# Kernel optimization log

Hardware: AMD Instinct MI355X
Metric: run time of the kernel (lower is better)

Reference implementation:

```python
import jax, jax.numpy as jnp
import numpy as np

COST_CLASS = 1.0
COST_COORD = 1.0
ALPHA = 0.25
GAMMA = 2.0
EPS = 1e-8
B, N = 4, 512


def setup_inputs() -> dict:
    key = jax.random.key(0)
    k1, k2, k3 = jax.random.split(key, 3)
    return {
        "pred_logits": jax.random.normal(k1, (B, N), dtype=jnp.float32),
        "pred_points": jax.random.uniform(k2, (B, N, 2), dtype=jnp.float32),
        "gt_points": jax.random.uniform(k3, (B, N, 2), dtype=jnp.float32),
        "gt_mask": jnp.ones((B, N), dtype=bool),
    }


def _cost_matrix(pred_logits, pred_points, gt_points):
    # focal-style classification cost, depends only on the prediction -> column-constant
    prob = jax.nn.sigmoid(pred_logits)                       # [B, N]
    neg = (1.0 - ALPHA) * prob ** GAMMA * (-jnp.log(1.0 - prob + EPS))
    pos = ALPHA * (1.0 - prob) ** GAMMA * (-jnp.log(prob + EPS))
    cost_class = (pos - neg)[:, :, None]                     # [B, N, 1]
    # L1 cdist between pred_points and gt_points
    cost_coord = jnp.sum(
        jnp.abs(pred_points[:, :, None, :] - gt_points[:, None, :, :]), axis=-1
    )                                                        # [B, N, N]
    return COST_CLASS * cost_class + COST_COORD * cost_coord


def _lsa(cost):
    # Jonker-Volgenant shortest augmenting path (e-maxx Hungarian), square, minimization.
    c = np.asarray(cost, dtype=np.float64)
    n = c.shape[0]
    INF = 1e18
    u = np.zeros(n + 1)
    v = np.zeros(n + 1)
    p = np.zeros(n + 1, dtype=np.int64)   # p[j] = row matched to column j (1-based)
    way = np.zeros(n + 1, dtype=np.int64)
    for i in range(1, n + 1):
        p[0] = i
        j0 = 0
        minv = np.full(n + 1, INF)
        used = np.zeros(n + 1, dtype=bool)
        while True:
            used[j0] = True
            i0 = p[j0]
            cur = c[i0 - 1] - u[i0] - v[1:]
            nu = ~used[1:]
            mv = minv[1:]
            wy = way[1:]
            upd = nu & (cur < mv)
            mv[upd] = cur[upd]
            wy[upd] = j0
            cand = np.where(nu, mv, INF)
            j1 = int(np.argmin(cand)) + 1
            delta = cand[j1 - 1]
            u[p[used]] += delta
            v[used] -= delta
            mv[nu] -= delta
            j0 = j1
            if p[j0] == 0:
                break
        while j0:
            j1 = int(way[j0])
            p[j0] = int(p[j1])
            j0 = j1
    col_of_row = np.empty(n, dtype=np.int64)
    col_of_row[p[1:] - 1] = np.arange(n)
    return np.arange(n), col_of_row


def reference(pred_logits, pred_points, gt_points, gt_mask):
    C = _cost_matrix(pred_logits, pred_points, gt_points)   # [B, N, N]
    mask = np.asarray(gt_mask)
    assert mask.all(), "reference assumes all gt slots valid (static shapes)"
    Cn = np.asarray(jax.device_get(C))
    pred_idx, gt_idx = [], []
    for b in range(Cn.shape[0]):
        r, c = _lsa(Cn[b])
        pred_idx.append(r)
        gt_idx.append(c)
    pred_idx = jnp.asarray(np.stack(pred_idx))
    gt_idx = jnp.asarray(np.stack(gt_idx))
    return pred_idx, gt_idx, C
```

## Files before the change

kernel.cpp:

```cpp
#include <hip/hip_runtime.h>
#include <math.h>

constexpr int B_ = 4;
constexpr int N_ = 512;

__device__ __forceinline__ float cephes_expf(float xin) {
#pragma clang fp contract(off)
    float x = fminf(xin, 88.3762626647950f);
    x = fmaxf(x, -88.3762626647949f);
    float fx = x * 1.44269504088896341f;
    fx = fx + 0.5f;
    fx = floorf(fx);
    float tmp = fx * 0.693359375f;
    float z0  = fx * -2.12194440e-4f;
    float r = x - tmp;
    r = r - z0;
    float zz = r * r;
    float y = 1.9875691500E-4f;
    y = y * r + 1.3981999507E-3f;
    y = y * r + 8.3334519073E-3f;
    y = y * r + 4.1665795894E-2f;
    y = y * r + 1.6666665459E-1f;
    y = y * r + 5.0000001201E-1f;
    y = y * zz + r;
    y = y + 1.0f;
    int n = (int)fx;
    float p2n = __uint_as_float((unsigned)(n + 0x7f) << 23);
    float res = y * p2n;
    return fmaxf(res, xin);
}

__device__ __forceinline__ float cephes_logf(float t) {
#pragma clang fp contract(off)
    float xx = fmaxf(t, 1.17549435e-38f);
    unsigned u = __float_as_uint(xx);
    int e_i = (int)(u >> 23) - 0x7f;
    float e = (float)e_i + 1.0f;
    float m = __uint_as_float((u & 0x807fffffu) | 0x3f000000u);
    int mask = (m < 0.707106781186547524f);
    float tmp1 = mask ? m : 0.0f;
    float x = m - 1.0f;
    e = e - (mask ? 1.0f : 0.0f);
    x = x + tmp1;
    float z = x * x;
    float y = 7.0376836292E-2f;
    y = y * x + -1.1514610310E-1f;
    y = y * x + 1.1676998740E-1f;
    y = y * x + -1.2420140846E-1f;
    y = y * x + 1.4249322787E-1f;
    y = y * x + -1.6668057665E-1f;
    y = y * x + 2.0000714765E-1f;
    y = y * x + -2.4999993993E-1f;
    y = y * x + 3.3333331174E-1f;
    y = y * x;
    y = y * z;
    y = e * -2.12194440e-4f + y;
    y = y - z * 0.5f;
    float res = x + y;
    res = res + e * 0.693359375f;
    return res;
}

__global__ __launch_bounds__(256) void class_cost_kernel(
    const float* __restrict__ logits, float* __restrict__ cc_out)
{
#pragma clang fp contract(off)
    int idx = blockIdx.x * 256 + threadIdx.x;
    if (idx >= B_ * N_) return;
    float x    = logits[idx];
    float e    = cephes_expf(-x);
    float prob = 1.0f / (1.0f + e);
    float om   = 1.0f - prob;
    float p2   = prob * prob;
    float o2   = om * om;
    float lneg = cephes_logf(om   + 1e-8f);
    float lpos = cephes_logf(prob + 1e-8f);
    float neg  = (0.75f * p2) * (-lneg);
    float pos  = (0.25f * o2) * (-lpos);
    cc_out[idx] = pos - neg;
}

__global__ __launch_bounds__(512) void cost_kernel(
    const float* __restrict__ cc,
    const float* __restrict__ pred_pts,
    const float* __restrict__ gt_pts,
    float* __restrict__ C)
{
    int blk = blockIdx.x;
    int b = blk >> 9;
    int i = blk & (N_ - 1);
    int j = threadIdx.x;

    const float2* pp2 = reinterpret_cast<const float2*>(pred_pts);
    const float2* gp2 = reinterpret_cast<const float2*>(gt_pts);
    float2 pp = pp2[b * N_ + i];
    float2 gp = gp2[b * N_ + j];
    float coord = fabsf(pp.x - gp.x) + fabsf(pp.y - gp.y);

    C[(size_t)b * N_ * N_ + (size_t)i * N_ + j] = cc[blk] + coord;
}

template<int CTRL>
__device__ __forceinline__ uint32_t dpp32(uint32_t x) {
    return (uint32_t)__builtin_amdgcn_update_dpp((int)x, (int)x, CTRL, 0xF, 0xF, false);
}

__device__ __forceinline__ uint64_t f64_key(double d) {
    uint64_t b = (uint64_t)__double_as_longlong(d);
    return b ^ ((b >> 63) ? 0xFFFFFFFFFFFFFFFFull : 0x8000000000000000ull);
}

__device__ __forceinline__ double readlane_f64(double d, int lane) {
    unsigned long long ll = (unsigned long long)__double_as_longlong(d);
    unsigned lo = (unsigned)__builtin_amdgcn_readlane((int)(unsigned)ll, lane);
    unsigned hi = (unsigned)__builtin_amdgcn_readlane((int)(unsigned)(ll >> 32), lane);
    return __longlong_as_double((long long)(((unsigned long long)hi << 32) | lo));
}

#define VSTEP(CTRL) {                                                          \
    uint32_t lo_o = dpp32<CTRL>(klo);                                          \
    uint32_t hi_o = dpp32<CTRL>(khi);                                          \
    uint64_t ko = ((uint64_t)hi_o << 32) | lo_o;                               \
    uint64_t kc = ((uint64_t)khi  << 32) | klo;                                \
    bool lt = (ko < kc);                                                       \
    klo = lt ? lo_o : klo; khi = lt ? hi_o : khi;                              \
}

__global__ __launch_bounds__(64) void solve_kernel(
    const float* __restrict__ C,
    float* __restrict__ pred_idx,
    float* __restrict__ gt_idx)
{
    const int b = blockIdx.x;
    const int t = threadIdx.x;
    const float*  Cs  = C + (size_t)b * N_ * N_;
    const float4* rp0 = reinterpret_cast<const float4*>(Cs);

    float4 pa = rp0[2 * t];
    float4 pb = rp0[2 * t + 1];

    {
        float w0 = 0.f, w1 = 0.f, w2 = 0.f, w3 = 0.f,
              w4 = 0.f, w5 = 0.f, w6 = 0.f, w7 = 0.f;
        for (int it = 0; it < 128; it += 8) {
            w0 += Cs[(t + 64 * (it + 0)) * 32];
            w1 += Cs[(t + 64 * (it + 1)) * 32];
            w2 += Cs[(t + 64 * (it + 2)) * 32];
            w3 += Cs[(t + 64 * (it + 3)) * 32];
            w4 += Cs[(t + 64 * (it + 4)) * 32];
            w5 += Cs[(t + 64 * (it + 5)) * 32];
            w6 += Cs[(t + 64 * (it + 6)) * 32];
            w7 += Cs[(t + 64 * (it + 7)) * 32];
        }
        float wsum = ((w0 + w1) + (w2 + w3)) + ((w4 + w5) + (w6 + w7));
        __asm__ volatile("" : : "v"(wsum));
    }

    double u0=0.0,u1=0.0,u2=0.0,u3=0.0,u4=0.0,u5=0.0,u6=0.0,u7=0.0;
    double v0=0.0,v1=0.0,v2=0.0,v3=0.0,v4=0.0,v5=0.0,v6=0.0,v7=0.0;
    int    p0=-1,p1=-1,p2=-1,p3=-1,p4=-1,p5=-1,p6=-1,p7=-1;

    #pragma unroll
    for (int k = 0; k < 8; ++k)
        pred_idx[b * N_ + t + 64 * k] = (float)(t + 64 * k);

    auto read_u_at = [&](int r) -> double {
        int sl = r & 7, ln = r >> 3;
        double x0 = (sl & 1) ? u1 : u0;
        double x1 = (sl & 1) ? u3 : u2;
        double x2 = (sl & 1) ? u5 : u4;
        double x3 = (sl & 1) ? u7 : u6;
        double y0 = (sl & 2) ? x1 : x0;
        double y1 = (sl & 2) ? x3 : x2;
        double z  = (sl & 4) ? y1 : y0;
        return readlane_f64(z, ln);
    };

    for (int i = 0; i < N_; ++i) {
        unsigned used_m  = 0u;
        unsigned chain_m = (t == (i >> 3)) ? (1u << (i & 7)) : 0u;
        double urow = read_u_at(i);
        float4 ca = pa, cb = pb;

        {
            int nxt = (i + 1 < N_) ? (i + 1) : i;
            const float4* rpn = rp0 + (nxt << 7);
            pa = rpn[2 * t];
            pb = rpn[2 * t + 1];
        }

        for (;;) {
            uint64_t q0 = (used_m & 0x01u) ? ~0ull : f64_key(((double)ca.x - urow) - v0);
            uint64_t q1 = (used_m & 0x02u) ? ~0ull : f64_key(((double)ca.y - urow) - v1);
            uint64_t q2 = (used_m & 0x04u) ? ~0ull : f64_key(((double)ca.z - urow) - v2);
            uint64_t q3 = (used_m & 0x08u) ? ~0ull : f64_key(((double)ca.w - urow) - v3);
            uint64_t q4 = (used_m & 0x10u) ? ~0ull : f64_key(((double)cb.x - urow) - v4);
            uint64_t q5 = (used_m & 0x20u) ? ~0ull : f64_key(((double)cb.y - urow) - v5);
            uint64_t q6 = (used_m & 0x40u) ? ~0ull : f64_key(((double)cb.z - urow) - v6);
            uint64_t q7 = (used_m & 0x80u) ? ~0ull : f64_key(((double)cb.w - urow) - v7);

            uint64_t ka = (q1 < q0) ? q1 : q0;  uint32_t sa = (q1 < q0) ? 1u : 0u;
            uint64_t kb = (q3 < q2) ? q3 : q2;  uint32_t sb = (q3 < q2) ? 3u : 2u;
            uint64_t kx = (q5 < q4) ? q5 : q4;  uint32_t sx = (q5 < q4) ? 5u : 4u;
            uint64_t kd = (q7 < q6) ? q7 : q6;  uint32_t sd = (q7 < q6) ? 7u : 6u;
            uint64_t ke = (kb < ka) ? kb : ka;  uint32_t se = (kb < ka) ? sb : sa;
            uint64_t kf = (kd < kx) ? kd : kx;  uint32_t sf = (kd < kx) ? sd : sx;
            uint64_t bk = (kf < ke) ? kf : ke;  uint32_t bslot = (kf < ke) ? sf : se;

            uint32_t klo = (uint32_t)bk, khi = (uint32_t)(bk >> 32);
            VSTEP(0x111) VSTEP(0x112) VSTEP(0x114)
            VSTEP(0x118) VSTEP(0x142) VSTEP(0x143)
            uint32_t Mlo = (uint32_t)__builtin_amdgcn_readlane((int)klo, 63);
            uint32_t Mhi = (uint32_t)__builtin_amdgcn_readlane((int)khi, 63);
            uint64_t M = ((uint64_t)Mhi << 32) | Mlo;

            unsigned long long tied = __ballot(bk == M);
            int lane1 = (int)__builtin_ctzll(tied);
            int slot1 = __builtin_amdgcn_readlane((int)bslot, lane1);

            int a0 = (slot1 & 1) ? p1 : p0;
            int a1 = (slot1 & 1) ? p3 : p2;
            int a2 = (slot1 & 1) ? p5 : p4;
            int a3 = (slot1 & 1) ? p7 : p6;
            int b0 = (slot1 & 2) ? a1 : a0;
            int b1 = (slot1 & 2) ? a3 : a2;
            int zz = (slot1 & 4) ? b1 : b0;
            int owner = __builtin_amdgcn_readlane(zz, lane1);

            uint64_t db = (M >> 63) ? (M ^ 0x8000000000000000ull) : ~M;
            double delta = __longlong_as_double((long long)db);

            if (owner < 0) {
                u0 += (chain_m & 0x01u) ? delta : 0.0;
                u1 += (chain_m & 0x02u) ? delta : 0.0;
                u2 += (chain_m & 0x04u) ? delta : 0.0;
                u3 += (chain_m & 0x08u) ? delta : 0.0;
                u4 += (chain_m & 0x10u) ? delta : 0.0;
                u5 += (chain_m & 0x20u) ? delta : 0.0;
                u6 += (chain_m & 0x40u) ? delta : 0.0;
                u7 += (chain_m & 0x80u) ? delta : 0.0;
                v0 -= (used_m  & 0x01u) ? delta : 0.0;
                v1 -= (used_m  & 0x02u) ? delta : 0.0;
                v2 -= (used_m  & 0x04u) ? delta : 0.0;
                v3 -= (used_m  & 0x08u) ? delta : 0.0;
                v4 -= (used_m  & 0x10u) ? delta : 0.0;
                v5 -= (used_m  & 0x20u) ? delta : 0.0;
                v6 -= (used_m  & 0x40u) ? delta : 0.0;
                v7 -= (used_m  & 0x80u) ? delta : 0.0;
                bool mine = (t == lane1);
                p0 = (mine && slot1 == 0) ? i : p0;
                p1 = (mine && slot1 == 1) ? i : p1;
                p2 = (mine && slot1 == 2) ? i : p2;
                p3 = (mine && slot1 == 3) ? i : p3;
                p4 = (mine && slot1 == 4) ? i : p4;
                p5 = (mine && slot1 == 5) ? i : p5;
                p6 = (mine && slot1 == 6) ? i : p6;
                p7 = (mine && slot1 == 7) ? i : p7;
                break;
            }

            {
                const float4* rp = rp0 + (owner << 7);
                ca = rp[2 * t];
                cb = rp[2 * t + 1];
            }
            urow = read_u_at(owner);

            u0 += (chain_m & 0x01u) ? delta : 0.0;
            u1 += (chain_m & 0x02u) ? delta : 0.0;
            u2 += (chain_m & 0x04u) ? delta : 0.0;
            u3 += (chain_m & 0x08u) ? delta : 0.0;
            u4 += (chain_m & 0x10u) ? delta : 0.0;
            u5 += (chain_m & 0x20u) ? delta : 0.0;
            u6 += (chain_m & 0x40u) ? delta : 0.0;
            u7 += (chain_m & 0x80u) ? delta : 0.0;
            v0 -= (used_m  & 0x01u) ? delta : 0.0;
            v1 -= (used_m  & 0x02u) ? delta : 0.0;
            v2 -= (used_m  & 0x04u) ? delta : 0.0;
            v3 -= (used_m  & 0x08u) ? delta : 0.0;
            v4 -= (used_m  & 0x10u) ? delta : 0.0;
            v5 -= (used_m  & 0x20u) ? delta : 0.0;
            v6 -= (used_m  & 0x40u) ? delta : 0.0;
            v7 -= (used_m  & 0x80u) ? delta : 0.0;

            used_m  |= (t == lane1)        ? (1u << slot1)       : 0u;
            chain_m |= (t == (owner >> 3)) ? (1u << (owner & 7)) : 0u;
        }
    }

    const int j0 = t << 3;
    gt_idx[b * N_ + p0] = (float)(j0);
    gt_idx[b * N_ + p1] = (float)(j0 + 1);
    gt_idx[b * N_ + p2] = (float)(j0 + 2);
    gt_idx[b * N_ + p3] = (float)(j0 + 3);
    gt_idx[b * N_ + p4] = (float)(j0 + 4);
    gt_idx[b * N_ + p5] = (float)(j0 + 5);
    gt_idx[b * N_ + p6] = (float)(j0 + 6);
    gt_idx[b * N_ + p7] = (float)(j0 + 7);
}

extern "C" void kernel_launch(void* const* d_in, const int* in_sizes, int n_in,
                              void* d_out, int out_size, void* d_ws, size_t ws_size,
                              hipStream_t stream)
{
    const float* logits   = (const float*)d_in[0];
    const float* pred_pts = (const float*)d_in[1];
    const float* gt_pts   = (const float*)d_in[2];

    float* out      = (float*)d_out;
    float* pred_idx = out;
    float* gt_idx   = out + B_ * N_;
    float* C        = out + 2 * B_ * N_;
    float* cc       = (float*)d_ws;

    class_cost_kernel<<<(B_ * N_ + 255) / 256, 256, 0, stream>>>(logits, cc);
    cost_kernel<<<B_ * N_, N_, 0, stream>>>(cc, pred_pts, gt_pts, C);
    solve_kernel<<<B_, 64, 0, stream>>>(C, pred_idx, gt_idx);
}
```

Before: 2.036 ms.

## Recompute cost rows in registers inside solver and use 32-bit two-stage wave min

```diff
diff --git a/kernel.cpp b/kernel.cpp
--- a/kernel.cpp
+++ b/kernel.cpp
@@ -104,10 +104,12 @@
 __device__ __forceinline__ uint32_t dpp32(uint32_t x) {
     return (uint32_t)__builtin_amdgcn_update_dpp((int)x, (int)x, CTRL, 0xF, 0xF, false);
 }
-
-__device__ __forceinline__ uint64_t f64_key(double d) {
-    uint64_t b = (uint64_t)__double_as_longlong(d);
-    return b ^ ((b >> 63) ? 0xFFFFFFFFFFFFFFFFull : 0x8000000000000000ull);
+#define UMINSTEP(X, CTRL) { uint32_t o_ = dpp32<CTRL>(X); X = (o_ < X) ? o_ : X; }
+
+__device__ __forceinline__ uint32_t wave_umin_lane63(uint32_t x) {
+    UMINSTEP(x, 0x111) UMINSTEP(x, 0x112) UMINSTEP(x, 0x114)
+    UMINSTEP(x, 0x118) UMINSTEP(x, 0x142) UMINSTEP(x, 0x143)
+    return x;
 }
 
 __device__ __forceinline__ double readlane_f64(double d, int lane) {
@@ -117,44 +119,27 @@
     return __longlong_as_double((long long)(((unsigned long long)hi << 32) | lo));
 }
 
-#define VSTEP(CTRL) {                                                          \
-    uint32_t lo_o = dpp32<CTRL>(klo);                                          \
-    uint32_t hi_o = dpp32<CTRL>(khi);                                          \
-    uint64_t ko = ((uint64_t)hi_o << 32) | lo_o;                               \
-    uint64_t kc = ((uint64_t)khi  << 32) | klo;                                \
-    bool lt = (ko < kc);                                                       \
-    klo = lt ? lo_o : klo; khi = lt ? hi_o : khi;                              \
-}
-
 __global__ __launch_bounds__(64) void solve_kernel(
-    const float* __restrict__ C,
+    const float* __restrict__ cc_in,
+    const float* __restrict__ pred_pts,
+    const float* __restrict__ gt_pts,
     float* __restrict__ pred_idx,
     float* __restrict__ gt_idx)
 {
     const int b = blockIdx.x;
     const int t = threadIdx.x;
-    const float*  Cs  = C + (size_t)b * N_ * N_;
-    const float4* rp0 = reinterpret_cast<const float4*>(Cs);
-
-    float4 pa = rp0[2 * t];
-    float4 pb = rp0[2 * t + 1];
-
-    {
-        float w0 = 0.f, w1 = 0.f, w2 = 0.f, w3 = 0.f,
-              w4 = 0.f, w5 = 0.f, w6 = 0.f, w7 = 0.f;
-        for (int it = 0; it < 128; it += 8) {
-            w0 += Cs[(t + 64 * (it + 0)) * 32];
-            w1 += Cs[(t + 64 * (it + 1)) * 32];
-            w2 += Cs[(t + 64 * (it + 2)) * 32];
-            w3 += Cs[(t + 64 * (it + 3)) * 32];
-            w4 += Cs[(t + 64 * (it + 4)) * 32];
-            w5 += Cs[(t + 64 * (it + 5)) * 32];
-            w6 += Cs[(t + 64 * (it + 6)) * 32];
-            w7 += Cs[(t + 64 * (it + 7)) * 32];
-        }
-        float wsum = ((w0 + w1) + (w2 + w3)) + ((w4 + w5) + (w6 + w7));
-        __asm__ volatile("" : : "v"(wsum));
-    }
+
+    const float2* pq = reinterpret_cast<const float2*>(pred_pts) + b * N_;
+    const float2* gq = reinterpret_cast<const float2*>(gt_pts)   + b * N_;
+    const float*  cq = cc_in + b * N_;
+    const int base = t << 3;
+
+    float2 r0 = pq[base + 0], r1 = pq[base + 1], r2 = pq[base + 2], r3 = pq[base + 3];
+    float2 r4 = pq[base + 4], r5 = pq[base + 5], r6 = pq[base + 6], r7 = pq[base + 7];
+    float2 g0 = gq[base + 0], g1 = gq[base + 1], g2 = gq[base + 2], g3 = gq[base + 3];
+    float2 g4 = gq[base + 4], g5 = gq[base + 5], g6 = gq[base + 6], g7 = gq[base + 7];
+    float  c0 = cq[base + 0], c1 = cq[base + 1], c2 = cq[base + 2], c3 = cq[base + 3];
+    float  c4 = cq[base + 4], c5 = cq[base + 5], c6 = cq[base + 6], c7 = cq[base + 7];
 
     double u0=0.0,u1=0.0,u2=0.0,u3=0.0,u4=0.0,u5=0.0,u6=0.0,u7=0.0;
     double v0=0.0,v1=0.0,v2=0.0,v3=0.0,v4=0.0,v5=0.0,v6=0.0,v7=0.0;
@@ -164,69 +149,108 @@
     for (int k = 0; k < 8; ++k)
         pred_idx[b * N_ + t + 64 * k] = (float)(t + 64 * k);
 
-    auto read_u_at = [&](int r) -> double {
-        int sl = r & 7, ln = r >> 3;
-        double x0 = (sl & 1) ? u1 : u0;
-        double x1 = (sl & 1) ? u3 : u2;
-        double x2 = (sl & 1) ? u5 : u4;
-        double x3 = (sl & 1) ? u7 : u6;
-        double y0 = (sl & 2) ? x1 : x0;
-        double y1 = (sl & 2) ? x3 : x2;
-        double z  = (sl & 4) ? y1 : y0;
-        return readlane_f64(z, ln);
-    };
+    #define SEL8F(sl, x0,x1,x2,x3,x4,x5,x6,x7, out) {                      \
+        float a0_=((sl)&1)?(x1):(x0), a1_=((sl)&1)?(x3):(x2);              \
+        float a2_=((sl)&1)?(x5):(x4), a3_=((sl)&1)?(x7):(x6);              \
+        float b0_=((sl)&2)?a1_:a0_,   b1_=((sl)&2)?a3_:a2_;                \
+        out = ((sl)&4)?b1_:b0_; }
+    #define SEL8I(sl, x0,x1,x2,x3,x4,x5,x6,x7, out) {                      \
+        int a0_=((sl)&1)?(x1):(x0), a1_=((sl)&1)?(x3):(x2);                \
+        int a2_=((sl)&1)?(x5):(x4), a3_=((sl)&1)?(x7):(x6);                \
+        int b0_=((sl)&2)?a1_:a0_,   b1_=((sl)&2)?a3_:a2_;                  \
+        out = ((sl)&4)?b1_:b0_; }
+    #define SEL8D(sl, x0,x1,x2,x3,x4,x5,x6,x7, out) {                      \
+        double a0_=((sl)&1)?(x1):(x0), a1_=((sl)&1)?(x3):(x2);             \
+        double a2_=((sl)&1)?(x5):(x4), a3_=((sl)&1)?(x7):(x6);             \
+        double b0_=((sl)&2)?a1_:a0_,   b1_=((sl)&2)?a3_:a2_;               \
+        out = ((sl)&4)?b1_:b0_; }
+
+    float px_r, py_r, cc_r; double urow;
+    #define ROW_SCALARS(r) {                                               \
+        int sl_ = (r) & 7, ln_ = (r) >> 3;                                 \
+        float sx_, sy_, sc_; double su_;                                   \
+        SEL8F(sl_, r0.x,r1.x,r2.x,r3.x,r4.x,r5.x,r6.x,r7.x, sx_);          \
+        SEL8F(sl_, r0.y,r1.y,r2.y,r3.y,r4.y,r5.y,r6.y,r7.y, sy_);          \
+        SEL8F(sl_, c0,c1,c2,c3,c4,c5,c6,c7, sc_);                          \
+        SEL8D(sl_, u0,u1,u2,u3,u4,u5,u6,u7, su_);                          \
+        px_r = __uint_as_float((unsigned)__builtin_amdgcn_readlane(        \
+                   (int)__float_as_uint(sx_), ln_));                       \
+        py_r = __uint_as_float((unsigned)__builtin_amdgcn_readlane(        \
+                   (int)__float_as_uint(sy_), ln_));                       \
+        cc_r = __uint_as_float((unsigned)__builtin_amdgcn_readlane(        \
+                   (int)__float_as_uint(sc_), ln_));                       \
+        urow = readlane_f64(su_, ln_); }
+
+    const float INF32 = __uint_as_float(0x7F800000u);
 
     for (int i = 0; i < N_; ++i) {
         unsigned used_m  = 0u;
         unsigned chain_m = (t == (i >> 3)) ? (1u << (i & 7)) : 0u;
-        double urow = read_u_at(i);
-        float4 ca = pa, cb = pb;
-
-        {
-            int nxt = (i + 1 < N_) ? (i + 1) : i;
-            const float4* rpn = rp0 + (nxt << 7);
-            pa = rpn[2 * t];
-            pb = rpn[2 * t + 1];
-        }
+        ROW_SCALARS(i);
 
         for (;;) {
-            uint64_t q0 = (used_m & 0x01u) ? ~0ull : f64_key(((double)ca.x - urow) - v0);
-            uint64_t q1 = (used_m & 0x02u) ? ~0ull : f64_key(((double)ca.y - urow) - v1);
-            uint64_t q2 = (used_m & 0x04u) ? ~0ull : f64_key(((double)ca.z - urow) - v2);
-            uint64_t q3 = (used_m & 0x08u) ? ~0ull : f64_key(((double)ca.w - urow) - v3);
-            uint64_t q4 = (used_m & 0x10u) ? ~0ull : f64_key(((double)cb.x - urow) - v4);
-            uint64_t q5 = (used_m & 0x20u) ? ~0ull : f64_key(((double)cb.y - urow) - v5);
-            uint64_t q6 = (used_m & 0x40u) ? ~0ull : f64_key(((double)cb.z - urow) - v6);
-            uint64_t q7 = (used_m & 0x80u) ? ~0ull : f64_key(((double)cb.w - urow) - v7);
-
-            uint64_t ka = (q1 < q0) ? q1 : q0;  uint32_t sa = (q1 < q0) ? 1u : 0u;
-            uint64_t kb = (q3 < q2) ? q3 : q2;  uint32_t sb = (q3 < q2) ? 3u : 2u;
-            uint64_t kx = (q5 < q4) ? q5 : q4;  uint32_t sx = (q5 < q4) ? 5u : 4u;
-            uint64_t kd = (q7 < q6) ? q7 : q6;  uint32_t sd = (q7 < q6) ? 7u : 6u;
-            uint64_t ke = (kb < ka) ? kb : ka;  uint32_t se = (kb < ka) ? sb : sa;
-            uint64_t kf = (kd < kx) ? kd : kx;  uint32_t sf = (kd < kx) ? sd : sx;
-            uint64_t bk = (kf < ke) ? kf : ke;  uint32_t bslot = (kf < ke) ? sf : se;
-
-            uint32_t klo = (uint32_t)bk, khi = (uint32_t)(bk >> 32);
-            VSTEP(0x111) VSTEP(0x112) VSTEP(0x114)
-            VSTEP(0x118) VSTEP(0x142) VSTEP(0x143)
-            uint32_t Mlo = (uint32_t)__builtin_amdgcn_readlane((int)klo, 63);
-            uint32_t Mhi = (uint32_t)__builtin_amdgcn_readlane((int)khi, 63);
+#pragma clang fp contract(off)
+            float w0 = cc_r + (fabsf(px_r - g0.x) + fabsf(py_r - g0.y));
+            float w1 = cc_r + (fabsf(px_r - g1.x) + fabsf(py_r - g1.y));
+            float w2 = cc_r + (fabsf(px_r - g2.x) + fabsf(py_r - g2.y));
+            float w3 = cc_r + (fabsf(px_r - g3.x) + fabsf(py_r - g3.y));
+            float w4 = cc_r + (fabsf(px_r - g4.x) + fabsf(py_r - g4.y));
+            float w5 = cc_r + (fabsf(px_r - g5.x) + fabsf(py_r - g5.y));
+            float w6 = cc_r + (fabsf(px_r - g6.x) + fabsf(py_r - g6.y));
+            float w7 = cc_r + (fabsf(px_r - g7.x) + fabsf(py_r - g7.y));
+            w0 = (used_m & 0x01u) ? INF32 : w0;
+            w1 = (used_m & 0x02u) ? INF32 : w1;
+            w2 = (used_m & 0x04u) ? INF32 : w2;
+            w3 = (used_m & 0x08u) ? INF32 : w3;
+            w4 = (used_m & 0x10u) ? INF32 : w4;
+            w5 = (used_m & 0x20u) ? INF32 : w5;
+            w6 = (used_m & 0x40u) ? INF32 : w6;
+            w7 = (used_m & 0x80u) ? INF32 : w7;
+
+            double d0 = ((double)w0 - urow) - v0;
+            double d1 = ((double)w1 - urow) - v1;
+            double d2 = ((double)w2 - urow) - v2;
+            double d3 = ((double)w3 - urow) - v3;
+            double d4 = ((double)w4 - urow) - v4;
+            double d5 = ((double)w5 - urow) - v5;
+            double d6 = ((double)w6 - urow) - v6;
+            double d7 = ((double)w7 - urow) - v7;
+
+            double  ka = (d1 < d0) ? d1 : d0;  uint32_t sa = (d1 < d0) ? 1u : 0u;
+            double  kb = (d3 < d2) ? d3 : d2;  uint32_t sb = (d3 < d2) ? 3u : 2u;
+            double  kx = (d5 < d4) ? d5 : d4;  uint32_t sx = (d5 < d4) ? 5u : 4u;
+            double  kd = (d7 < d6) ? d7 : d6;  uint32_t sd = (d7 < d6) ? 7u : 6u;
+            double  ke = (kb < ka) ? kb : ka;  uint32_t se = (kb < ka) ? sb : sa;
+            double  kf = (kd < kx) ? kd : kx;  uint32_t sf = (kd < kx) ? sd : sx;
+            double  bv = (kf < ke) ? kf : ke;  uint32_t bslot = (kf < ke) ? sf : se;
+
+            uint64_t kb64 = (uint64_t)__double_as_longlong(bv);
+            kb64 ^= (kb64 >> 63) ? 0xFFFFFFFFFFFFFFFFull : 0x8000000000000000ull;
+            uint32_t khi = (uint32_t)(kb64 >> 32);
+            uint32_t klo = (uint32_t)kb64;
+
+            int own_pre;
+            SEL8I(bslot, p0,p1,p2,p3,p4,p5,p6,p7, own_pre);
+
+            uint32_t Mhi = (uint32_t)__builtin_amdgcn_readlane(
+                               (int)wave_umin_lane63(khi), 63);
+            unsigned long long tied_hi = __ballot(khi == Mhi);
+
+            int lane1; uint32_t Mlo;
+            if (__builtin_popcountll(tied_hi) == 1) {
+                lane1 = (int)__builtin_ctzll(tied_hi);
+                Mlo = (uint32_t)__builtin_amdgcn_readlane((int)klo, lane1);
+            } else {
+                uint32_t kl2 = (khi == Mhi) ? klo : 0xFFFFFFFFu;
+                Mlo = (uint32_t)__builtin_amdgcn_readlane(
+                          (int)wave_umin_lane63(kl2), 63);
+                lane1 = (int)__builtin_ctzll(__ballot(khi == Mhi && klo == Mlo));
+            }
+
+            int slot1 = __builtin_amdgcn_readlane((int)bslot, lane1);
+            int owner = __builtin_amdgcn_readlane(own_pre, lane1);
+
             uint64_t M = ((uint64_t)Mhi << 32) | Mlo;
-
-            unsigned long long tied = __ballot(bk == M);
-            int lane1 = (int)__builtin_ctzll(tied);
-            int slot1 = __builtin_amdgcn_readlane((int)bslot, lane1);
-
-            int a0 = (slot1 & 1) ? p1 : p0;
-            int a1 = (slot1 & 1) ? p3 : p2;
-            int a2 = (slot1 & 1) ? p5 : p4;
-            int a3 = (slot1 & 1) ? p7 : p6;
-            int b0 = (slot1 & 2) ? a1 : a0;
-            int b1 = (slot1 & 2) ? a3 : a2;
-            int zz = (slot1 & 4) ? b1 : b0;
-            int owner = __builtin_amdgcn_readlane(zz, lane1);
-
             uint64_t db = (M >> 63) ? (M ^ 0x8000000000000000ull) : ~M;
             double delta = __longlong_as_double((long long)db);
 
@@ -259,12 +283,7 @@
                 break;
             }
 
-            {
-                const float4* rp = rp0 + (owner << 7);
-                ca = rp[2 * t];
-                cb = rp[2 * t + 1];
-            }
-            urow = read_u_at(owner);
+            ROW_SCALARS(owner);
 
             u0 += (chain_m & 0x01u) ? delta : 0.0;
             u1 += (chain_m & 0x02u) ? delta : 0.0;
@@ -288,15 +307,14 @@
         }
     }
 
-    const int j0 = t << 3;
-    gt_idx[b * N_ + p0] = (float)(j0);
-    gt_idx[b * N_ + p1] = (float)(j0 + 1);
-    gt_idx[b * N_ + p2] = (float)(j0 + 2);
-    gt_idx[b * N_ + p3] = (float)(j0 + 3);
-    gt_idx[b * N_ + p4] = (float)(j0 + 4);
-    gt_idx[b * N_ + p5] = (float)(j0 + 5);
-    gt_idx[b * N_ + p6] = (float)(j0 + 6);
-    gt_idx[b * N_ + p7] = (float)(j0 + 7);
+    gt_idx[b * N_ + p0] = (float)(base);
+    gt_idx[b * N_ + p1] = (float)(base + 1);
+    gt_idx[b * N_ + p2] = (float)(base + 2);
+    gt_idx[b * N_ + p3] = (float)(base + 3);
+    gt_idx[b * N_ + p4] = (float)(base + 4);
+    gt_idx[b * N_ + p5] = (float)(base + 5);
+    gt_idx[b * N_ + p6] = (float)(base + 6);
+    gt_idx[b * N_ + p7] = (float)(base + 7);
 }
 
 extern "C" void kernel_launch(void* const* d_in, const int* in_sizes, int n_in,
@@ -315,5 +333,5 @@
 
     class_cost_kernel<<<(B_ * N_ + 255) / 256, 256, 0, stream>>>(logits, cc);
     cost_kernel<<<B_ * N_, N_, 0, stream>>>(cc, pred_pts, gt_pts, C);
-    solve_kernel<<<B_, 64, 0, stream>>>(C, pred_idx, gt_idx);
-}
+    solve_kernel<<<B_, 64, 0, stream>>>(cc, pred_pts, gt_pts, pred_idx, gt_idx);
+}
```

Measured after the change: 1.647 ms, median of 3. 1.24x faster.
